# Kernel tuning notes

Hardware: AMD Instinct MI355X
Metric: run time of the kernel (lower is better)

Reference implementation:

```python
import math
import jax, jax.numpy as jnp
import numpy as np

N, L, H, E, K = 4, 768, 8, 64, 1  # batch, seq (L==S), heads, feat, num_sines


def setup_inputs() -> dict:
    key = jax.random.key(0)
    ks = jax.random.split(key, 8)
    queries = jax.random.normal(ks[0], (N, L, H, E), jnp.float32)
    keys = jax.random.normal(ks[1], (N, L, H, E), jnp.float32)
    values = jax.random.normal(ks[2], (N, L, H, E), jnp.float32)
    attn_mask_add = jnp.zeros((L, L), jnp.float32)
    key_lengths_add = jnp.zeros((N, L), jnp.float32)
    freqs = jax.random.normal(ks[3], (H, E, K), jnp.float32) - 4.0  # init shift
    offsets = jax.random.normal(ks[4], (H, E, K), jnp.float32)
    gains = jax.random.normal(ks[5], (H, E, K), jnp.float32)
    # gains.data /= sqrt(||gains||_{-1}) / 2
    gains = gains / (jnp.sqrt(jnp.linalg.norm(gains, axis=-1, keepdims=True)) / 2.0)
    gate = jax.random.normal(ks[6], (H, E), jnp.float32)
    return dict(queries=queries, keys=keys, values=values,
                attn_mask_add=attn_mask_add, key_lengths_add=key_lengths_add,
                freqs=freqs, offsets=offsets, gains=gains, gate=gate)


def reference(queries, keys, values, attn_mask_add, key_lengths_add,
              freqs, offsets, gains, gate):
    n, l, h, e = queries.shape
    softmax_temp = 1.0 / math.sqrt(e)
    positions = jnp.arange(l, dtype=queries.dtype)  # (L,)
    f = jax.nn.sigmoid(freqs)[None] / 2.0  # (1,H,E,K)
    phases_q = 2.0 * math.pi * f * positions[:, None, None, None] + offsets[None]
    phases_k = 2.0 * math.pi * f * positions[:, None, None, None]
    # interleave cos/sin along last dim -> (L,H,E,2K)
    omega_q = jnp.stack([jnp.cos(phases_q), jnp.sin(phases_q)], axis=-1).reshape(l, h, e, 2 * f.shape[-1])
    omega_k = jnp.stack([jnp.cos(phases_k), jnp.sin(phases_k)], axis=-1).reshape(l, h, e, 2 * f.shape[-1])
    g = jax.nn.softplus(gains)
    g2 = jnp.stack([g, g], axis=-1).reshape(h, e, 2 * f.shape[-1])  # (H,E,2K)
    # positional kernel P: (L,S,H,E)
    P = jnp.einsum('lhdk,hdk,shdk->lshd', omega_q, g2 ** 2, omega_k)
    P = (1.0 - gate) * P + gate  # gated
    QK = jnp.einsum('nlhd,lshd,nshd->nhls', queries, P, keys)
    QK = QK + attn_mask_add[None, None] + key_lengths_add[:, None, None, :]
    A = jax.nn.softmax(softmax_temp * QK, axis=-1)
    V = jnp.einsum('nhls,nshd->nlhd', A, values)
    return V
```

## Files before the change

### kernel.cpp

```cpp
#include <hip/hip_runtime.h>
#include <math.h>
#include <stdint.h>

#define NB 4
#define LQ 768
#define NH 8
#define NE 64
#define ND 192
#define TEMP 0.125f

typedef _Float16 f16;
typedef __attribute__((ext_vector_type(8))) _Float16 f16x8;
typedef __attribute__((ext_vector_type(4))) float f32x4;

__device__ __forceinline__ void stage16(f16* lds_base, const f16* g, int lane) {
#if __has_builtin(__builtin_amdgcn_global_load_lds)
    __builtin_amdgcn_global_load_lds(
        (const __attribute__((address_space(1))) uint32_t*)g,
        (__attribute__((address_space(3))) uint32_t*)lds_base, 16, 0, 0);
#else
    *(uint4*)((char*)lds_base + lane * 16) = *(const uint4*)g;
#endif
}

__global__ __launch_bounds__(256) void sinattn_prep(
    const float* __restrict__ Q, const float* __restrict__ K,
    const float* __restrict__ freqs, const float* __restrict__ offsets,
    const float* __restrict__ gains, const float* __restrict__ gate,
    f16* __restrict__ Qf, f16* __restrict__ Kf)
{
    int idx = blockIdx.x * 256 + threadIdx.x;
    int eg = idx & 7, e0 = eg << 3;
    int h  = (idx >> 3) & 7;
    int t  = idx >> 6;
    int l  = t % LQ;
    int n  = t / LQ;
    int nh = (n << 3) | h;
    int he = (h << 6) | e0;

    const float* qp = Q + (size_t)idx * 8;
    const float* kp = K + (size_t)idx * 8;
    float4 q0 = *(const float4*)qp, q1 = *(const float4*)(qp + 4);
    float4 k0 = *(const float4*)kp, k1 = *(const float4*)(kp + 4);
    float qv[8] = {q0.x,q0.y,q0.z,q0.w, q1.x,q1.y,q1.z,q1.w};
    float kv[8] = {k0.x,k0.y,k0.z,k0.w, k1.x,k1.y,k1.z,k1.w};

    float4 fA = *(const float4*)(freqs   + he), fB = *(const float4*)(freqs   + he + 4);
    float4 oA = *(const float4*)(offsets + he), oB = *(const float4*)(offsets + he + 4);
    float4 gA = *(const float4*)(gains   + he), gB = *(const float4*)(gains   + he + 4);
    float4 tA = *(const float4*)(gate    + he), tB = *(const float4*)(gate    + he + 4);
    float fv[8] = {fA.x,fA.y,fA.z,fA.w, fB.x,fB.y,fB.z,fB.w};
    float ov[8] = {oA.x,oA.y,oA.z,oA.w, oB.x,oB.y,oB.z,oB.w};
    float gv[8] = {gA.x,gA.y,gA.z,gA.w, gB.x,gB.y,gB.z,gB.w};
    float tv[8] = {tA.x,tA.y,tA.z,tA.w, tB.x,tB.y,tB.z,tB.w};

    f16x8 oq0, oq1, oq2, ok0, ok1, ok2;
    float lf = (float)l;
    #pragma unroll
    for (int j = 0; j < 8; ++j) {
        float f  = 0.5f / (1.0f + __expf(-fv[j]));
        float gn = gv[j];
        float sp = (gn > 15.0f) ? gn : __logf(1.0f + __expf(gn));
        float gt = tv[j];
        float a  = (1.0f - gt) * sp * sp;
        float fh = __uint_as_float(__float_as_uint(f) & 0xFFFFF000u);
        float fl = f - fh;
        float t0 = lf * fh;
        float tr = t0 - floorf(t0);
        tr = __builtin_fmaf(lf, fl, tr);
        float pk = 6.28318530717958647f * tr;
        float pq = pk + ov[j];
        float sq = __sinf(pq), cq = __cosf(pq);
        float sk = __sinf(pk), ck = __cosf(pk);
        oq0[j] = (f16)(qv[j] * a * cq);
        oq1[j] = (f16)(qv[j] * a * sq);
        oq2[j] = (f16)(qv[j] * gt);
        ok0[j] = (f16)(kv[j] * ck);
        ok1[j] = (f16)(kv[j] * sk);
        ok2[j] = (f16)(kv[j]);
    }
    size_t base = ((size_t)nh * LQ + l) * ND + e0;
    *(f16x8*)(Qf + base)            = oq0;
    *(f16x8*)(Qf + base + NE)       = oq1;
    *(f16x8*)(Qf + base + 2 * NE)   = oq2;
    *(f16x8*)(Kf + base)            = ok0;
    *(f16x8*)(Kf + base + NE)       = ok1;
    *(f16x8*)(Kf + base + 2 * NE)   = ok2;
}

__global__ __launch_bounds__(256) void sinattn_vt(
    const float* __restrict__ V, f16* __restrict__ Vt)
{
    __shared__ f16 tile[64][72];
    int b = blockIdx.x;
    int st = b % 12, nh = b / 12;
    int n = nh >> 3, h = nh & 7;
    int s0 = st * 64;
    int tid = threadIdx.x;

    int sl = tid >> 2, e0 = (tid & 3) << 4;
    const float4* vp = (const float4*)(V + ((size_t)(n * LQ + s0 + sl) * NH + h) * NE + e0);
    float4 a0 = vp[0], a1 = vp[1], a2 = vp[2], a3 = vp[3];
    float vv[16] = { a0.x,a0.y,a0.z,a0.w, a1.x,a1.y,a1.z,a1.w,
                     a2.x,a2.y,a2.z,a2.w, a3.x,a3.y,a3.z,a3.w };
    #pragma unroll
    for (int j = 0; j < 16; ++j) tile[e0 + j][sl] = (f16)vv[j];
    __syncthreads();

    int er = tid >> 2, sc = tid & 3;
    f16* op = Vt + ((size_t)nh * NE + er) * LQ + s0 + sc * 16;
    *(uint4*)op       = *(const uint4*)&tile[er][sc * 16];
    *(uint4*)(op + 8) = *(const uint4*)&tile[er][sc * 16 + 8];
}

__global__ __launch_bounds__(256, 2) void sinattn_flash(
    const f16* __restrict__ Qf, const f16* __restrict__ Kf, const f16* __restrict__ Vt,
    const float* __restrict__ mask, const float* __restrict__ keylen,
    float* __restrict__ out)
{
    __shared__ __attribute__((aligned(16))) f16 sK[2][64 * 24 * 8];
    __shared__ __attribute__((aligned(16))) f16 sV[2][64 * 8 * 8];
    __shared__ __attribute__((aligned(16))) f16 sP[4][16 * 72];

    int tid  = threadIdx.x;
    int wv   = tid >> 6;
    int lane = tid & 63;
    int grp  = lane >> 4;
    int r16  = lane & 15;
    int swz  = r16 & 7;

    int bid = blockIdx.x;
    int nh  = bid & 31;
    int lt  = bid >> 5;
    int n   = nh >> 3;
    int l0  = lt * 64;

    f16x8 qf[6];
    {
        size_t rbase = ((size_t)nh * LQ + l0 + wv * 16 + r16) * ND + grp * 8;
        #pragma unroll
        for (int d0 = 0; d0 < 6; ++d0)
            qf[d0] = *(const f16x8*)(Qf + rbase + d0 * 32);
    }

    int goffK[6], goffV[2];
    #pragma unroll
    for (int i = 0; i < 6; ++i) {
        int p = i * 256 + wv * 64 + lane;
        int r = p / 24, c = p - r * 24;
        int cl = (c & ~7) | ((c & 7) ^ (r & 7));
        goffK[i] = r * ND + cl * 8;
    }
    #pragma unroll
    for (int i = 0; i < 2; ++i) {
        int p = i * 256 + wv * 64 + lane;
        int r = p >> 3, c = p & 7;
        goffV[i] = r * LQ + (c ^ (r & 7)) * 8;
    }
    const f16* Kb = Kf + (size_t)nh * LQ * ND;
    const f16* Vb = Vt + (size_t)nh * NE * LQ;

    {
        #pragma unroll
        for (int i = 0; i < 6; ++i)
            stage16(&sK[0][(i * 256 + wv * 64) * 8], Kb + goffK[i], lane);
        #pragma unroll
        for (int i = 0; i < 2; ++i)
            stage16(&sV[0][(i * 256 + wv * 64) * 8], Vb + goffV[i], lane);
    }

    float m_i[4], l_i[4];
    f32x4 O[4];
    #pragma unroll
    for (int rr = 0; rr < 4; ++rr) { m_i[rr] = -INFINITY; l_i[rr] = 0.f; }
    #pragma unroll
    for (int tt = 0; tt < 4; ++tt)
        #pragma unroll
        for (int rr = 0; rr < 4; ++rr) O[tt][rr] = 0.f;

    for (int c = 0; c < 12; ++c) {
        int cur = c & 1;
        int s0  = c * 64;
        __syncthreads();

        if (c < 11) {
            const f16* kg = Kb + (s0 + 64) * ND;
            const f16* vg = Vb + (s0 + 64);
            #pragma unroll
            for (int i = 0; i < 6; ++i)
                stage16(&sK[cur ^ 1][(i * 256 + wv * 64) * 8], kg + goffK[i], lane);
            #pragma unroll
            for (int i = 0; i < 2; ++i)
                stage16(&sV[cur ^ 1][(i * 256 + wv * 64) * 8], vg + goffV[i], lane);
        }

        float klv[4], mreg[4][4];
        #pragma unroll
        for (int j = 0; j < 4; ++j) klv[j] = keylen[n * LQ + s0 + j * 16 + r16];
        #pragma unroll
        for (int rr = 0; rr < 4; ++rr) {
            int lrow = l0 + wv * 16 + grp * 4 + rr;
            #pragma unroll
            for (int j = 0; j < 4; ++j)
                mreg[rr][j] = mask[lrow * LQ + s0 + j * 16 + r16];
        }

        f32x4 st[4];
        #pragma unroll
        for (int j = 0; j < 4; ++j)
            #pragma unroll
            for (int rr = 0; rr < 4; ++rr) st[j][rr] = 0.f;
        #pragma unroll
        for (int d0 = 0; d0 < 6; ++d0) {
            #pragma unroll
            for (int j = 0; j < 4; ++j) {
                int cc = d0 * 4 + grp;
                int cl = (cc & ~7) | ((cc & 7) ^ swz);
                f16x8 bf = *(const f16x8*)&sK[cur][((j * 16 + r16) * 24 + cl) * 8];
                st[j] = __builtin_amdgcn_mfma_f32_16x16x32_f16(qf[d0], bf, st[j], 0, 0, 0);
            }
        }

        #pragma unroll
        for (int rr = 0; rr < 4; ++rr) {
            float lg[4];
            float mx = -INFINITY;
            #pragma unroll
            for (int j = 0; j < 4; ++j) {
                lg[j] = TEMP * (st[j][rr] + mreg[rr][j] + klv[j]);
                mx = fmaxf(mx, lg[j]);
            }
            #pragma unroll
            for (int d = 1; d < 16; d <<= 1) mx = fmaxf(mx, __shfl_xor(mx, d));
            float mnew  = fmaxf(m_i[rr], mx);
            float alpha = __expf(m_i[rr] - mnew);
            float rs = 0.f;
            #pragma unroll
            for (int j = 0; j < 4; ++j) {
                float p = __expf(lg[j] - mnew);
                rs += p;
                sP[wv][(grp * 4 + rr) * 72 + j * 16 + r16] = (f16)p;
            }
            #pragma unroll
            for (int d = 1; d < 16; d <<= 1) rs += __shfl_xor(rs, d);
            l_i[rr] = l_i[rr] * alpha + rs;
            m_i[rr] = mnew;
            #pragma unroll
            for (int tt = 0; tt < 4; ++tt) O[tt][rr] *= alpha;
        }

        #pragma unroll
        for (int kk = 0; kk < 2; ++kk) {
            f16x8 pa = *(const f16x8*)&sP[wv][r16 * 72 + kk * 32 + grp * 8];
            #pragma unroll
            for (int tt = 0; tt < 4; ++tt) {
                int cc = kk * 4 + grp;
                f16x8 vb = *(const f16x8*)&sV[cur][((tt * 16 + r16) * 8 + (cc ^ swz)) * 8];
                O[tt] = __builtin_amdgcn_mfma_f32_16x16x32_f16(pa, vb, O[tt], 0, 0, 0);
            }
        }
    }

    #pragma unroll
    for (int rr = 0; rr < 4; ++rr) {
        float inv = 1.0f / l_i[rr];
        int lrow = l0 + wv * 16 + grp * 4 + rr;
        float* op = out + ((size_t)(n * LQ + lrow) * NH + (nh & 7)) * NE;
        #pragma unroll
        for (int tt = 0; tt < 4; ++tt)
            op[tt * 16 + r16] = O[tt][rr] * inv;
    }
}

extern "C" void kernel_launch(void* const* d_in, const int* in_sizes, int n_in,
                              void* d_out, int out_size, void* d_ws, size_t ws_size,
                              hipStream_t stream)
{
    const float* Q      = (const float*)d_in[0];
    const float* K      = (const float*)d_in[1];
    const float* V      = (const float*)d_in[2];
    const float* mask   = (const float*)d_in[3];
    const float* keylen = (const float*)d_in[4];
    const float* freqs  = (const float*)d_in[5];
    const float* offs   = (const float*)d_in[6];
    const float* gains  = (const float*)d_in[7];
    const float* gate   = (const float*)d_in[8];
    float* out = (float*)d_out;

    const size_t P = (size_t)NB * NH * LQ * ND;
    f16* Qf = (f16*)d_ws;
    f16* Kf = Qf + P;
    f16* Vt = Kf + P;

    sinattn_prep<<<768, 256, 0, stream>>>(Q, K, freqs, offs, gains, gate, Qf, Kf);
    sinattn_vt<<<384, 256, 0, stream>>>(V, Vt);
    sinattn_flash<<<NB * NH * (LQ / 64), 256, 0, stream>>>(Qf, Kf, Vt,
                                                           mask, keylen, out);
}
```

Baseline: 122.3 us.

## Fuse prep and V-transpose kernels, shrink flash tiles, load V directly

Merges the Q/K feature prep and the V transpose into one launch, which saves one kernel launch. The flash kernel moves to 3 waves with 48-row query tiles, so the grid grows to 512 blocks for better CU coverage. V is now read straight from global memory into registers instead of being staged in LDS, and the softmax row sums are computed with an MFMA against a ones vector in place of shuffle reductions. The softmax temperature is folded into Q at prep time. Direct V loads may raise global latency, and the smaller tiles lower K reuse per block.

After: 124.3 us. Within noise of the previous version (+1.7%).

```diff
diff --git a/kernel.cpp b/kernel.cpp
--- a/kernel.cpp
+++ b/kernel.cpp
@@ -23,107 +23,106 @@
 #endif
 }
 
-__global__ __launch_bounds__(256) void sinattn_prep(
+__global__ __launch_bounds__(256) void sinattn_prepvt(
     const float* __restrict__ Q, const float* __restrict__ K,
+    const float* __restrict__ V,
     const float* __restrict__ freqs, const float* __restrict__ offsets,
     const float* __restrict__ gains, const float* __restrict__ gate,
-    f16* __restrict__ Qf, f16* __restrict__ Kf)
+    f16* __restrict__ Qf, f16* __restrict__ Kf, f16* __restrict__ Vt)
 {
-    int idx = blockIdx.x * 256 + threadIdx.x;
-    int eg = idx & 7, e0 = eg << 3;
-    int h  = (idx >> 3) & 7;
-    int t  = idx >> 6;
-    int l  = t % LQ;
-    int n  = t / LQ;
-    int nh = (n << 3) | h;
-    int he = (h << 6) | e0;
-
-    const float* qp = Q + (size_t)idx * 8;
-    const float* kp = K + (size_t)idx * 8;
-    float4 q0 = *(const float4*)qp, q1 = *(const float4*)(qp + 4);
-    float4 k0 = *(const float4*)kp, k1 = *(const float4*)(kp + 4);
-    float qv[8] = {q0.x,q0.y,q0.z,q0.w, q1.x,q1.y,q1.z,q1.w};
-    float kv[8] = {k0.x,k0.y,k0.z,k0.w, k1.x,k1.y,k1.z,k1.w};
-
-    float4 fA = *(const float4*)(freqs   + he), fB = *(const float4*)(freqs   + he + 4);
-    float4 oA = *(const float4*)(offsets + he), oB = *(const float4*)(offsets + he + 4);
-    float4 gA = *(const float4*)(gains   + he), gB = *(const float4*)(gains   + he + 4);
-    float4 tA = *(const float4*)(gate    + he), tB = *(const float4*)(gate    + he + 4);
-    float fv[8] = {fA.x,fA.y,fA.z,fA.w, fB.x,fB.y,fB.z,fB.w};
-    float ov[8] = {oA.x,oA.y,oA.z,oA.w, oB.x,oB.y,oB.z,oB.w};
-    float gv[8] = {gA.x,gA.y,gA.z,gA.w, gB.x,gB.y,gB.z,gB.w};
-    float tv[8] = {tA.x,tA.y,tA.z,tA.w, tB.x,tB.y,tB.z,tB.w};
-
-    f16x8 oq0, oq1, oq2, ok0, ok1, ok2;
-    float lf = (float)l;
-    #pragma unroll
-    for (int j = 0; j < 8; ++j) {
-        float f  = 0.5f / (1.0f + __expf(-fv[j]));
-        float gn = gv[j];
-        float sp = (gn > 15.0f) ? gn : __logf(1.0f + __expf(gn));
-        float gt = tv[j];
-        float a  = (1.0f - gt) * sp * sp;
-        float fh = __uint_as_float(__float_as_uint(f) & 0xFFFFF000u);
-        float fl = f - fh;
-        float t0 = lf * fh;
-        float tr = t0 - floorf(t0);
-        tr = __builtin_fmaf(lf, fl, tr);
-        float pk = 6.28318530717958647f * tr;
-        float pq = pk + ov[j];
-        float sq = __sinf(pq), cq = __cosf(pq);
-        float sk = __sinf(pk), ck = __cosf(pk);
-        oq0[j] = (f16)(qv[j] * a * cq);
-        oq1[j] = (f16)(qv[j] * a * sq);
-        oq2[j] = (f16)(qv[j] * gt);
-        ok0[j] = (f16)(kv[j] * ck);
-        ok1[j] = (f16)(kv[j] * sk);
-        ok2[j] = (f16)(kv[j]);
-    }
-    size_t base = ((size_t)nh * LQ + l) * ND + e0;
-    *(f16x8*)(Qf + base)            = oq0;
-    *(f16x8*)(Qf + base + NE)       = oq1;
-    *(f16x8*)(Qf + base + 2 * NE)   = oq2;
-    *(f16x8*)(Kf + base)            = ok0;
-    *(f16x8*)(Kf + base + NE)       = ok1;
-    *(f16x8*)(Kf + base + 2 * NE)   = ok2;
-}
-
-__global__ __launch_bounds__(256) void sinattn_vt(
-    const float* __restrict__ V, f16* __restrict__ Vt)
-{
-    __shared__ f16 tile[64][72];
-    int b = blockIdx.x;
-    int st = b % 12, nh = b / 12;
-    int n = nh >> 3, h = nh & 7;
-    int s0 = st * 64;
-    int tid = threadIdx.x;
-
-    int sl = tid >> 2, e0 = (tid & 3) << 4;
-    const float4* vp = (const float4*)(V + ((size_t)(n * LQ + s0 + sl) * NH + h) * NE + e0);
-    float4 a0 = vp[0], a1 = vp[1], a2 = vp[2], a3 = vp[3];
-    float vv[16] = { a0.x,a0.y,a0.z,a0.w, a1.x,a1.y,a1.z,a1.w,
-                     a2.x,a2.y,a2.z,a2.w, a3.x,a3.y,a3.z,a3.w };
-    #pragma unroll
-    for (int j = 0; j < 16; ++j) tile[e0 + j][sl] = (f16)vv[j];
-    __syncthreads();
-
-    int er = tid >> 2, sc = tid & 3;
-    f16* op = Vt + ((size_t)nh * NE + er) * LQ + s0 + sc * 16;
-    *(uint4*)op       = *(const uint4*)&tile[er][sc * 16];
-    *(uint4*)(op + 8) = *(const uint4*)&tile[er][sc * 16 + 8];
-}
-
-__global__ __launch_bounds__(256, 2) void sinattn_flash(
+    if (blockIdx.x < 768) {
+        int idx = blockIdx.x * 256 + threadIdx.x;
+        int eg = idx & 7, e0 = eg << 3;
+        int h  = (idx >> 3) & 7;
+        int t  = idx >> 6;
+        int l  = t % LQ;
+        int n  = t / LQ;
+        int nh = (n << 3) | h;
+        int he = (h << 6) | e0;
+
+        const float* qp = Q + (size_t)idx * 8;
+        const float* kp = K + (size_t)idx * 8;
+        float4 q0 = *(const float4*)qp, q1 = *(const float4*)(qp + 4);
+        float4 k0 = *(const float4*)kp, k1 = *(const float4*)(kp + 4);
+        float qv[8] = {q0.x,q0.y,q0.z,q0.w, q1.x,q1.y,q1.z,q1.w};
+        float kv[8] = {k0.x,k0.y,k0.z,k0.w, k1.x,k1.y,k1.z,k1.w};
+
+        float4 fA = *(const float4*)(freqs   + he), fB = *(const float4*)(freqs   + he + 4);
+        float4 oA = *(const float4*)(offsets + he), oB = *(const float4*)(offsets + he + 4);
+        float4 gA = *(const float4*)(gains   + he), gB = *(const float4*)(gains   + he + 4);
+        float4 tA = *(const float4*)(gate    + he), tB = *(const float4*)(gate    + he + 4);
+        float fv[8] = {fA.x,fA.y,fA.z,fA.w, fB.x,fB.y,fB.z,fB.w};
+        float ov[8] = {oA.x,oA.y,oA.z,oA.w, oB.x,oB.y,oB.z,oB.w};
+        float gv[8] = {gA.x,gA.y,gA.z,gA.w, gB.x,gB.y,gB.z,gB.w};
+        float tv[8] = {tA.x,tA.y,tA.z,tA.w, tB.x,tB.y,tB.z,tB.w};
+
+        f16x8 oq0, oq1, oq2, ok0, ok1, ok2;
+        float lf = (float)l;
+        #pragma unroll
+        for (int j = 0; j < 8; ++j) {
+            float f  = 0.5f / (1.0f + __expf(-fv[j]));
+            float gn = gv[j];
+            float sp = (gn > 15.0f) ? gn : __logf(1.0f + __expf(gn));
+            float gt = tv[j];
+            float a  = (1.0f - gt) * sp * sp;
+            float fh = __uint_as_float(__float_as_uint(f) & 0xFFFFF000u);
+            float fl = f - fh;
+            float t0 = lf * fh;
+            float tr = t0 - floorf(t0);
+            tr = __builtin_fmaf(lf, fl, tr);
+            float pk = 6.28318530717958647f * tr;
+            float pq = pk + ov[j];
+            float sq = __sinf(pq), cq = __cosf(pq);
+            float sk = __sinf(pk), ck = __cosf(pk);
+            oq0[j] = (f16)(qv[j] * a * cq * TEMP);
+            oq1[j] = (f16)(qv[j] * a * sq * TEMP);
+            oq2[j] = (f16)(qv[j] * gt * TEMP);
+            ok0[j] = (f16)(kv[j] * ck);
+            ok1[j] = (f16)(kv[j] * sk);
+            ok2[j] = (f16)(kv[j]);
+        }
+        size_t base = ((size_t)nh * LQ + l) * ND + e0;
+        *(f16x8*)(Qf + base)          = oq0;
+        *(f16x8*)(Qf + base + NE)     = oq1;
+        *(f16x8*)(Qf + base + 2*NE)   = oq2;
+        *(f16x8*)(Kf + base)          = ok0;
+        *(f16x8*)(Kf + base + NE)     = ok1;
+        *(f16x8*)(Kf + base + 2*NE)   = ok2;
+    } else {
+        __shared__ f16 tile[64][72];
+        int b = blockIdx.x - 768;
+        int st = b % 12, nh = b / 12;
+        int n = nh >> 3, h = nh & 7;
+        int s0 = st * 64;
+        int tid = threadIdx.x;
+
+        int sl = tid >> 2, e0 = (tid & 3) << 4;
+        const float4* vp = (const float4*)(V + ((size_t)(n * LQ + s0 + sl) * NH + h) * NE + e0);
+        float4 a0 = vp[0], a1 = vp[1], a2 = vp[2], a3 = vp[3];
+        float vv[16] = { a0.x,a0.y,a0.z,a0.w, a1.x,a1.y,a1.z,a1.w,
+                         a2.x,a2.y,a2.z,a2.w, a3.x,a3.y,a3.z,a3.w };
+        #pragma unroll
+        for (int j = 0; j < 16; ++j) tile[e0 + j][sl] = (f16)vv[j];
+        __syncthreads();
+
+        int er = tid >> 2, sc = tid & 3;
+        f16* op = Vt + ((size_t)nh * NE + er) * LQ + s0 + sc * 16;
+        *(uint4*)op       = *(const uint4*)&tile[er][sc * 16];
+        *(uint4*)(op + 8) = *(const uint4*)&tile[er][sc * 16 + 8];
+    }
+}
+
+__global__ __launch_bounds__(192, 2) void sinattn_flash(
     const f16* __restrict__ Qf, const f16* __restrict__ Kf, const f16* __restrict__ Vt,
     const float* __restrict__ mask, const float* __restrict__ keylen,
     float* __restrict__ out)
 {
     __shared__ __attribute__((aligned(16))) f16 sK[2][64 * 24 * 8];
-    __shared__ __attribute__((aligned(16))) f16 sV[2][64 * 8 * 8];
-    __shared__ __attribute__((aligned(16))) f16 sP[4][16 * 72];
+    __shared__ __attribute__((aligned(16))) f16 sP[3][16 * 68];
 
     int tid  = threadIdx.x;
     int wv   = tid >> 6;
+    int wvu  = __builtin_amdgcn_readfirstlane(wv);
     int lane = tid & 63;
     int grp  = lane >> 4;
     int r16  = lane & 15;
@@ -133,7 +132,23 @@
     int nh  = bid & 31;
     int lt  = bid >> 5;
     int n   = nh >> 3;
-    int l0  = lt * 64;
+    int l0  = lt * 48;
+
+    const f16* Kb = Kf + (size_t)nh * LQ * ND;
+    const f16* Vb = Vt + (size_t)nh * NE * LQ;
+
+    int goffK[8];
+    #pragma unroll
+    for (int i = 0; i < 8; ++i) {
+        int p = i * 192 + wv * 64 + lane;
+        int r = p / 24, c = p - r * 24;
+        int cl = (c & ~7) | ((c & 7) ^ (r & 7));
+        goffK[i] = r * ND + cl * 8;
+    }
+
+    #pragma unroll
+    for (int i = 0; i < 8; ++i)
+        stage16(&sK[0][(i * 192 + wvu * 64) * 8], Kb + goffK[i], lane);
 
     f16x8 qf[6];
     {
@@ -143,31 +158,9 @@
             qf[d0] = *(const f16x8*)(Qf + rbase + d0 * 32);
     }
 
-    int goffK[6], goffV[2];
-    #pragma unroll
-    for (int i = 0; i < 6; ++i) {
-        int p = i * 256 + wv * 64 + lane;
-        int r = p / 24, c = p - r * 24;
-        int cl = (c & ~7) | ((c & 7) ^ (r & 7));
-        goffK[i] = r * ND + cl * 8;
-    }
-    #pragma unroll
-    for (int i = 0; i < 2; ++i) {
-        int p = i * 256 + wv * 64 + lane;
-        int r = p >> 3, c = p & 7;
-        goffV[i] = r * LQ + (c ^ (r & 7)) * 8;
-    }
-    const f16* Kb = Kf + (size_t)nh * LQ * ND;
-    const f16* Vb = Vt + (size_t)nh * NE * LQ;
-
-    {
-        #pragma unroll
-        for (int i = 0; i < 6; ++i)
-            stage16(&sK[0][(i * 256 + wv * 64) * 8], Kb + goffK[i], lane);
-        #pragma unroll
-        for (int i = 0; i < 2; ++i)
-            stage16(&sV[0][(i * 256 + wv * 64) * 8], Vb + goffV[i], lane);
-    }
+    f16x8 ones;
+    #pragma unroll
+    for (int j = 0; j < 8; ++j) ones[j] = (f16)1.0f;
 
     float m_i[4], l_i[4];
     f32x4 O[4];
@@ -184,19 +177,16 @@
         __syncthreads();
 
         if (c < 11) {
-            const f16* kg = Kb + (s0 + 64) * ND;
-            const f16* vg = Vb + (s0 + 64);
-            #pragma unroll
-            for (int i = 0; i < 6; ++i)
-                stage16(&sK[cur ^ 1][(i * 256 + wv * 64) * 8], kg + goffK[i], lane);
-            #pragma unroll
-            for (int i = 0; i < 2; ++i)
-                stage16(&sV[cur ^ 1][(i * 256 + wv * 64) * 8], vg + goffV[i], lane);
-        }
-
-        float klv[4], mreg[4][4];
-        #pragma unroll
-        for (int j = 0; j < 4; ++j) klv[j] = keylen[n * LQ + s0 + j * 16 + r16];
+            const f16* kg = Kb + (size_t)(s0 + 64) * ND;
+            #pragma unroll
+            for (int i = 0; i < 8; ++i)
+                stage16(&sK[cur ^ 1][(i * 192 + wvu * 64) * 8], kg + goffK[i], lane);
+        }
+
+        float klv[4];
+        #pragma unroll
+        for (int j = 0; j < 4; ++j) klv[j] = TEMP * keylen[n * LQ + s0 + j * 16 + r16];
+        float mreg[4][4];
         #pragma unroll
         for (int rr = 0; rr < 4; ++rr) {
             int lrow = l0 + wv * 16 + grp * 4 + rr;
@@ -204,6 +194,13 @@
             for (int j = 0; j < 4; ++j)
                 mreg[rr][j] = mask[lrow * LQ + s0 + j * 16 + r16];
         }
+        f16x8 vb[2][4];
+        #pragma unroll
+        for (int kk = 0; kk < 2; ++kk)
+            #pragma unroll
+            for (int tt = 0; tt < 4; ++tt)
+                vb[kk][tt] = *(const f16x8*)(Vb + (size_t)(tt * 16 + r16) * LQ
+                                             + s0 + kk * 32 + grp * 8);
 
         f32x4 st[4];
         #pragma unroll
@@ -221,44 +218,44 @@
             }
         }
 
+        float alpha[4];
         #pragma unroll
         for (int rr = 0; rr < 4; ++rr) {
             float lg[4];
             float mx = -INFINITY;
             #pragma unroll
             for (int j = 0; j < 4; ++j) {
-                lg[j] = TEMP * (st[j][rr] + mreg[rr][j] + klv[j]);
+                lg[j] = __builtin_fmaf(TEMP, mreg[rr][j], st[j][rr] + klv[j]);
                 mx = fmaxf(mx, lg[j]);
             }
             #pragma unroll
             for (int d = 1; d < 16; d <<= 1) mx = fmaxf(mx, __shfl_xor(mx, d));
-            float mnew  = fmaxf(m_i[rr], mx);
-            float alpha = __expf(m_i[rr] - mnew);
-            float rs = 0.f;
-            #pragma unroll
-            for (int j = 0; j < 4; ++j) {
-                float p = __expf(lg[j] - mnew);
-                rs += p;
-                sP[wv][(grp * 4 + rr) * 72 + j * 16 + r16] = (f16)p;
-            }
-            #pragma unroll
-            for (int d = 1; d < 16; d <<= 1) rs += __shfl_xor(rs, d);
-            l_i[rr] = l_i[rr] * alpha + rs;
-            m_i[rr] = mnew;
-            #pragma unroll
-            for (int tt = 0; tt < 4; ++tt) O[tt][rr] *= alpha;
-        }
-
+            float mnew = fmaxf(m_i[rr], mx);
+            alpha[rr]  = __expf(m_i[rr] - mnew);
+            m_i[rr]    = mnew;
+            #pragma unroll
+            for (int j = 0; j < 4; ++j)
+                sP[wv][(grp * 4 + rr) * 68 + j * 16 + r16] = (f16)__expf(lg[j] - mnew);
+        }
+        #pragma unroll
+        for (int tt = 0; tt < 4; ++tt)
+            #pragma unroll
+            for (int rr = 0; rr < 4; ++rr) O[tt][rr] *= alpha[rr];
+
+        f32x4 rs;
+        #pragma unroll
+        for (int rr = 0; rr < 4; ++rr) rs[rr] = 0.f;
         #pragma unroll
         for (int kk = 0; kk < 2; ++kk) {
-            f16x8 pa = *(const f16x8*)&sP[wv][r16 * 72 + kk * 32 + grp * 8];
-            #pragma unroll
-            for (int tt = 0; tt < 4; ++tt) {
-                int cc = kk * 4 + grp;
-                f16x8 vb = *(const f16x8*)&sV[cur][((tt * 16 + r16) * 8 + (cc ^ swz)) * 8];
-                O[tt] = __builtin_amdgcn_mfma_f32_16x16x32_f16(pa, vb, O[tt], 0, 0, 0);
-            }
-        }
+            f16x8 pa = *(const f16x8*)&sP[wv][r16 * 68 + kk * 32 + grp * 8];
+            rs = __builtin_amdgcn_mfma_f32_16x16x32_f16(pa, ones, rs, 0, 0, 0);
+            #pragma unroll
+            for (int tt = 0; tt < 4; ++tt)
+                O[tt] = __builtin_amdgcn_mfma_f32_16x16x32_f16(pa, vb[kk][tt], O[tt], 0, 0, 0);
+        }
+        #pragma unroll
+        for (int rr = 0; rr < 4; ++rr)
+            l_i[rr] = __builtin_fmaf(l_i[rr], alpha[rr], rs[rr]);
     }
 
     #pragma unroll
@@ -292,8 +289,7 @@
     f16* Kf = Qf + P;
     f16* Vt = Kf + P;
 
-    sinattn_prep<<<768, 256, 0, stream>>>(Q, K, freqs, offs, gains, gate, Qf, Kf);
-    sinattn_vt<<<384, 256, 0, stream>>>(V, Vt);
-    sinattn_flash<<<NB * NH * (LQ / 64), 256, 0, stream>>>(Qf, Kf, Vt,
-                                                           mask, keylen, out);
-}
+    sinattn_prepvt<<<1152, 256, 0, stream>>>(Q, K, V, freqs, offs, gains, gate,
+                                             Qf, Kf, Vt);
+    sinattn_flash<<<512, 192, 0, stream>>>(Qf, Kf, Vt, mask, keylen, out);
+}
```
